# Optimization experiments

Hardware: AMD Instinct MI355X
Metric: run time of the kernel (lower is better)

## Reference

```python
import jax, jax.numpy as jnp
import numpy as np


def setup_inputs() -> dict:
    key = jax.random.key(0)
    k1, k2 = jax.random.split(key)
    B, Q, C, H, W = 2, 100, 151, 128, 128
    pred_logits = jax.random.normal(k1, (B, Q, C), dtype=jnp.float32)
    pred_masks = jax.random.normal(k2, (B, Q, H, W), dtype=jnp.float32)
    return {"pred_logits": pred_logits, "pred_masks": pred_masks, "out_size": 512}


def reference(pred_logits, pred_masks, out_size):
    B, Q, C = pred_logits.shape
    # class_scores[b,q,c] * mask_probs[b,q,h,w] summed over q == contraction bqc,bqhw->bchw
    class_scores = jax.nn.softmax(pred_logits, axis=-1)
    mask_probs = jax.nn.sigmoid(pred_masks)
    seg = jnp.einsum('bqc,bqhw->bchw', class_scores, mask_probs)
    seg = seg[:, 1:, :, :]  # drop background class 0
    # bilinear, half-pixel centers == torch align_corners=False
    seg = jax.image.resize(seg, (B, C - 1, out_size, out_size), method='bilinear')
    return seg
```

## Files before the change

kernel.cpp:

```cpp
#include <hip/hip_runtime.h>
#include <hip/hip_bf16.h>
#include <math.h>

#define NCLS 151
#define NQ   100
#define NB   2
#define HW   16384
#define NCO  150
#define OUTW 512
#define KPAD 128
#define CPAD 160
#define CBLK 32
#define AROW 136
#define BROW 72
#define SROW 130

using short8  = __attribute__((ext_vector_type(8))) short;
using short4v = __attribute__((ext_vector_type(4))) short;
using f32x4   = __attribute__((ext_vector_type(4))) float;

static __device__ __forceinline__ ushort f2bf(float x) {
    union { float f; unsigned u; } v; v.f = x;
    unsigned r = v.u + 0x7fff + ((v.u >> 16) & 1);
    return (ushort)(r >> 16);
}

__global__ __launch_bounds__(64) void softmax_k(const float* __restrict__ logits,
                                                ushort* __restrict__ scoresT) {
    int q = blockIdx.x & 127;
    int b = blockIdx.x >> 7;
    int lane = threadIdx.x;
    ushort* A = scoresT + (size_t)b * CPAD * KPAD;

    if (q >= NQ) {
        A[lane * KPAD + q] = 0;
        A[(lane + 64) * KPAD + q] = 0;
        if (lane < 32) A[(lane + 128) * KPAD + q] = 0;
        return;
    }

    const float* in = logits + (size_t)(b * NQ + q) * NCLS;
    float v0 = in[lane];
    float v1 = in[lane + 64];
    float v2 = (lane < NCLS - 128) ? in[lane + 128] : -1e30f;

    float m = fmaxf(fmaxf(v0, v1), v2);
    #pragma unroll
    for (int o = 32; o; o >>= 1) m = fmaxf(m, __shfl_xor(m, o));

    float e0 = __expf(v0 - m);
    float e1 = __expf(v1 - m);
    float e2 = (lane < NCLS - 128) ? __expf(v2 - m) : 0.f;

    float s = e0 + e1 + e2;
    #pragma unroll
    for (int o = 32; o; o >>= 1) s += __shfl_xor(s, o);

    float inv = 1.f / s;
    if (lane >= 1) A[(lane - 1) * KPAD + q] = f2bf(e0 * inv);
    A[(lane + 63) * KPAD + q] = f2bf(e1 * inv);
    if (lane < 23)       A[(lane + 127) * KPAD + q] = f2bf(e2 * inv);
    else if (lane < 33)  A[(lane + 127) * KPAD + q] = 0;
}

__global__ __launch_bounds__(512, 4) void fused_k(const float* __restrict__ masks,
                                                  const ushort* __restrict__ scoresT,
                                                  float* __restrict__ out) {
    __shared__ __align__(16) ushort s_a[CBLK][AROW];
    __shared__ __align__(16) char uni[256 * BROW * 2];
    ushort (*s_bt)[BROW] = (ushort(*)[BROW])uni;
    float* s_seg = (float*)uni;

    int r   = blockIdx.x;
    int b   = blockIdx.y / 5;
    int cs  = blockIdx.y % 5;
    int tid = threadIdx.x;
    int r1  = min(r + 1, 127);
    int wid = tid >> 6, lane = tid & 63;
    int pr = lane & 15, kg = lane >> 4;

    {
        const float4* asrc = (const float4*)(scoresT + (size_t)(b * CPAD + cs * CBLK) * KPAD);
        float4 av = asrc[tid];
        int c = tid >> 4, kc = tid & 15;
        *(float4*)&s_a[c][kc * 8] = av;
    }

    f32x4 acc[2][2];
    #pragma unroll
    for (int ct = 0; ct < 2; ++ct)
        #pragma unroll
        for (int nt = 0; nt < 2; ++nt) acc[ct][nt] = (f32x4){0.f, 0.f, 0.f, 0.f};

    const float* mb = masks + (size_t)b * NQ * HW;

    #pragma unroll
    for (int kc2 = 0; kc2 < 2; ++kc2) {
        #pragma unroll
        for (int i0 = 0; i0 < 4096; i0 += 512) {
            int i = i0 + tid;
            int p = i & 255, kk4 = i >> 8;
            int gpix = ((p < 128) ? r : r1) * 128 + (p & 127);
            short4v sv;
            #pragma unroll
            for (int e = 0; e < 4; ++e) {
                int gk = kc2 * 64 + kk4 * 4 + e;
                float s = 0.f;
                if (gk < NQ) {
                    float x = mb[(size_t)gk * HW + gpix];
                    s = 1.f / (1.f + __expf(-x));
                }
                sv[e] = (short)f2bf(s);
            }
            *(short4v*)&s_bt[p][kk4 * 4] = sv;
        }
        __syncthreads();

        #pragma unroll
        for (int ks = 0; ks < 2; ++ks) {
            short8 b0 = *(const short8*)&s_bt[wid * 32 + pr][ks * 32 + kg * 8];
            short8 b1 = *(const short8*)&s_bt[wid * 32 + 16 + pr][ks * 32 + kg * 8];
            #pragma unroll
            for (int ct = 0; ct < 2; ++ct) {
                short8 af = *(const short8*)&s_a[ct * 16 + pr][kc2 * 64 + ks * 32 + kg * 8];
                acc[ct][0] = __builtin_amdgcn_mfma_f32_16x16x32_bf16(af, b0, acc[ct][0], 0, 0, 0);
                acc[ct][1] = __builtin_amdgcn_mfma_f32_16x16x32_bf16(af, b1, acc[ct][1], 0, 0, 0);
            }
        }
        __syncthreads();
    }

    #pragma unroll
    for (int ct = 0; ct < 2; ++ct)
        #pragma unroll
        for (int nt = 0; nt < 2; ++nt) {
            int p = wid * 32 + nt * 16 + pr;
            int rs = p >> 7, px = p & 127;
            #pragma unroll
            for (int j = 0; j < 4; ++j) {
                int c = ct * 16 + kg * 4 + j;
                s_seg[(rs * CBLK + c) * SROW + px] = acc[ct][nt][j];
            }
        }
    __syncthreads();

    int cbase = cs * CBLK;
    for (int it = tid; it < CBLK * 128; it += 512) {
        int k = it & 127;
        int c = it >> 7;
        int cg = cbase + c;
        if (cg >= NCO) break;
        int km = max(k - 1, 0), kp = min(k + 1, 127);
        const float* s0 = &s_seg[c * SROW];
        const float* s1 = &s_seg[(CBLK + c) * SROW];
        float a0 = s0[km], a1 = s0[k], a2 = s0[kp];
        float b0 = s1[km], b1 = s1[k], b2 = s1[kp];

        float t0 = a0 + 0.625f * (a1 - a0);
        float t1 = a0 + 0.875f * (a1 - a0);
        float t2 = a1 + 0.125f * (a2 - a1);
        float t3 = a1 + 0.375f * (a2 - a1);
        float u0 = b0 + 0.625f * (b1 - b0);
        float u1 = b0 + 0.875f * (b1 - b0);
        float u2 = b1 + 0.125f * (b2 - b1);
        float u3 = b1 + 0.375f * (b2 - b1);

        float* op = out + (size_t)(b * NCO + cg) * (OUTW * OUTW) + 4 * k;

        if (r == 0) {
            f32x4 o = {t0, t1, t2, t3};
            __builtin_nontemporal_store(o, (f32x4*)(op));
            __builtin_nontemporal_store(o, (f32x4*)(op + OUTW));
        }
        int nr = (r == 127) ? 2 : 4;
        #pragma unroll
        for (int ri = 0; ri < 4; ++ri) {
            if (ri >= nr) break;
            float fh = 0.125f + 0.25f * (float)ri;
            int h = 4 * r + 2 + ri;
            f32x4 o;
            o.x = t0 + fh * (u0 - t0);
            o.y = t1 + fh * (u1 - t1);
            o.z = t2 + fh * (u2 - t2);
            o.w = t3 + fh * (u3 - t3);
            __builtin_nontemporal_store(o, (f32x4*)(op + (size_t)h * OUTW));
        }
    }
}

extern "C" void kernel_launch(void* const* d_in, const int* in_sizes, int n_in,
                              void* d_out, int out_size, void* d_ws, size_t ws_size,
                              hipStream_t stream) {
    const float* logits = (const float*)d_in[0];
    const float* masks  = (const float*)d_in[1];
    float* out = (float*)d_out;

    ushort* scoresT = (ushort*)d_ws;

    softmax_k<<<dim3(NB * 128), dim3(64), 0, stream>>>(logits, scoresT);
    fused_k<<<dim3(128, NB * 5), dim3(512), 0, stream>>>(masks, scoresT, out);
}
```

Measured before the change: 72.29 us.

## Compute sigmoid mask tile once per block and loop over all class chunks

Each block now loads and sigmoids the two mask rows for all 128 queries once, keeps them in LDS, and loops over the five class chunks internally, where previously five separate blocks each redid that load and sigmoid. This removes the 5x redundant global mask reads and transcendental work. In exchange the grid shrinks from 1280 to 256 blocks, LDS use per block grows (occupancy hint lowered to 2), and the output write phase is serialized within each block, which may reduce parallelism for the store-bound resize.

```diff
diff --git a/kernel.cpp b/kernel.cpp
--- a/kernel.cpp
+++ b/kernel.cpp
@@ -12,7 +12,7 @@
 #define CPAD 160
 #define CBLK 32
 #define AROW 136
-#define BROW 72
+#define BROW 136
 #define SROW 130
 
 using short8  = __attribute__((ext_vector_type(8))) short;
@@ -63,48 +63,42 @@
     else if (lane < 33)  A[(lane + 127) * KPAD + q] = 0;
 }
 
-__global__ __launch_bounds__(512, 4) void fused_k(const float* __restrict__ masks,
+__global__ __launch_bounds__(512, 2) void fused_k(const float* __restrict__ masks,
                                                   const ushort* __restrict__ scoresT,
                                                   float* __restrict__ out) {
-    __shared__ __align__(16) ushort s_a[CBLK][AROW];
-    __shared__ __align__(16) char uni[256 * BROW * 2];
-    ushort (*s_bt)[BROW] = (ushort(*)[BROW])uni;
-    float* s_seg = (float*)uni;
+    __shared__ __align__(16) ushort s_a[CPAD][AROW];
+    __shared__ __align__(16) ushort s_bt[256][BROW];
+    __shared__ float s_seg[2][CBLK][SROW];
 
     int r   = blockIdx.x;
-    int b   = blockIdx.y / 5;
-    int cs  = blockIdx.y % 5;
+    int b   = blockIdx.y;
     int tid = threadIdx.x;
     int r1  = min(r + 1, 127);
     int wid = tid >> 6, lane = tid & 63;
     int pr = lane & 15, kg = lane >> 4;
 
     {
-        const float4* asrc = (const float4*)(scoresT + (size_t)(b * CPAD + cs * CBLK) * KPAD);
-        float4 av = asrc[tid];
-        int c = tid >> 4, kc = tid & 15;
-        *(float4*)&s_a[c][kc * 8] = av;
-    }
-
-    f32x4 acc[2][2];
-    #pragma unroll
-    for (int ct = 0; ct < 2; ++ct)
-        #pragma unroll
-        for (int nt = 0; nt < 2; ++nt) acc[ct][nt] = (f32x4){0.f, 0.f, 0.f, 0.f};
-
-    const float* mb = masks + (size_t)b * NQ * HW;
-
-    #pragma unroll
-    for (int kc2 = 0; kc2 < 2; ++kc2) {
-        #pragma unroll
-        for (int i0 = 0; i0 < 4096; i0 += 512) {
+        const float4* asrc = (const float4*)(scoresT + (size_t)b * CPAD * KPAD);
+        #pragma unroll
+        for (int j = 0; j < 5; ++j) {
+            int i = tid + j * 512;
+            float4 v = asrc[i];
+            int c = i >> 4, kc = i & 15;
+            *(float4*)&s_a[c][kc * 8] = v;
+        }
+    }
+
+    {
+        const float* mb = masks + (size_t)b * NQ * HW;
+        #pragma unroll
+        for (int i0 = 0; i0 < 8192; i0 += 512) {
             int i = i0 + tid;
             int p = i & 255, kk4 = i >> 8;
             int gpix = ((p < 128) ? r : r1) * 128 + (p & 127);
             short4v sv;
             #pragma unroll
             for (int e = 0; e < 4; ++e) {
-                int gk = kc2 * 64 + kk4 * 4 + e;
+                int gk = kk4 * 4 + e;
                 float s = 0.f;
                 if (gk < NQ) {
                     float x = mb[(size_t)gk * HW + gpix];
@@ -114,76 +108,85 @@
             }
             *(short4v*)&s_bt[p][kk4 * 4] = sv;
         }
-        __syncthreads();
-
-        #pragma unroll
-        for (int ks = 0; ks < 2; ++ks) {
+    }
+    __syncthreads();
+
+    for (int cs = 0; cs < 5; ++cs) {
+        f32x4 acc[2][2];
+        #pragma unroll
+        for (int ct = 0; ct < 2; ++ct)
+            #pragma unroll
+            for (int nt = 0; nt < 2; ++nt) acc[ct][nt] = (f32x4){0.f, 0.f, 0.f, 0.f};
+
+        #pragma unroll
+        for (int ks = 0; ks < 4; ++ks) {
             short8 b0 = *(const short8*)&s_bt[wid * 32 + pr][ks * 32 + kg * 8];
             short8 b1 = *(const short8*)&s_bt[wid * 32 + 16 + pr][ks * 32 + kg * 8];
             #pragma unroll
             for (int ct = 0; ct < 2; ++ct) {
-                short8 af = *(const short8*)&s_a[ct * 16 + pr][kc2 * 64 + ks * 32 + kg * 8];
+                short8 af = *(const short8*)&s_a[cs * CBLK + ct * 16 + pr][ks * 32 + kg * 8];
                 acc[ct][0] = __builtin_amdgcn_mfma_f32_16x16x32_bf16(af, b0, acc[ct][0], 0, 0, 0);
                 acc[ct][1] = __builtin_amdgcn_mfma_f32_16x16x32_bf16(af, b1, acc[ct][1], 0, 0, 0);
             }
         }
+
         __syncthreads();
-    }
-
-    #pragma unroll
-    for (int ct = 0; ct < 2; ++ct)
-        #pragma unroll
-        for (int nt = 0; nt < 2; ++nt) {
-            int p = wid * 32 + nt * 16 + pr;
-            int rs = p >> 7, px = p & 127;
-            #pragma unroll
-            for (int j = 0; j < 4; ++j) {
-                int c = ct * 16 + kg * 4 + j;
-                s_seg[(rs * CBLK + c) * SROW + px] = acc[ct][nt][j];
-            }
-        }
-    __syncthreads();
-
-    int cbase = cs * CBLK;
-    for (int it = tid; it < CBLK * 128; it += 512) {
-        int k = it & 127;
-        int c = it >> 7;
-        int cg = cbase + c;
-        if (cg >= NCO) break;
-        int km = max(k - 1, 0), kp = min(k + 1, 127);
-        const float* s0 = &s_seg[c * SROW];
-        const float* s1 = &s_seg[(CBLK + c) * SROW];
-        float a0 = s0[km], a1 = s0[k], a2 = s0[kp];
-        float b0 = s1[km], b1 = s1[k], b2 = s1[kp];
-
-        float t0 = a0 + 0.625f * (a1 - a0);
-        float t1 = a0 + 0.875f * (a1 - a0);
-        float t2 = a1 + 0.125f * (a2 - a1);
-        float t3 = a1 + 0.375f * (a2 - a1);
-        float u0 = b0 + 0.625f * (b1 - b0);
-        float u1 = b0 + 0.875f * (b1 - b0);
-        float u2 = b1 + 0.125f * (b2 - b1);
-        float u3 = b1 + 0.375f * (b2 - b1);
-
-        float* op = out + (size_t)(b * NCO + cg) * (OUTW * OUTW) + 4 * k;
-
-        if (r == 0) {
-            f32x4 o = {t0, t1, t2, t3};
-            __builtin_nontemporal_store(o, (f32x4*)(op));
-            __builtin_nontemporal_store(o, (f32x4*)(op + OUTW));
-        }
-        int nr = (r == 127) ? 2 : 4;
-        #pragma unroll
-        for (int ri = 0; ri < 4; ++ri) {
-            if (ri >= nr) break;
-            float fh = 0.125f + 0.25f * (float)ri;
-            int h = 4 * r + 2 + ri;
-            f32x4 o;
-            o.x = t0 + fh * (u0 - t0);
-            o.y = t1 + fh * (u1 - t1);
-            o.z = t2 + fh * (u2 - t2);
-            o.w = t3 + fh * (u3 - t3);
-            __builtin_nontemporal_store(o, (f32x4*)(op + (size_t)h * OUTW));
+
+        #pragma unroll
+        for (int ct = 0; ct < 2; ++ct)
+            #pragma unroll
+            for (int nt = 0; nt < 2; ++nt) {
+                int p = wid * 32 + nt * 16 + pr;
+                int rs = p >> 7, px = p & 127;
+                #pragma unroll
+                for (int j = 0; j < 4; ++j) {
+                    int c = ct * 16 + kg * 4 + j;
+                    s_seg[rs][c][px] = acc[ct][nt][j];
+                }
+            }
+        __syncthreads();
+
+        int cbase = cs * CBLK;
+        for (int it = tid; it < CBLK * 128; it += 512) {
+            int k = it & 127;
+            int c = it >> 7;
+            int cg = cbase + c;
+            if (cg >= NCO) break;
+            int km = max(k - 1, 0), kp = min(k + 1, 127);
+            const float* s0 = s_seg[0][c];
+            const float* s1 = s_seg[1][c];
+            float a0 = s0[km], a1 = s0[k], a2 = s0[kp];
+            float b0 = s1[km], b1 = s1[k], b2 = s1[kp];
+
+            float t0 = a0 + 0.625f * (a1 - a0);
+            float t1 = a0 + 0.875f * (a1 - a0);
+            float t2 = a1 + 0.125f * (a2 - a1);
+            float t3 = a1 + 0.375f * (a2 - a1);
+            float u0 = b0 + 0.625f * (b1 - b0);
+            float u1 = b0 + 0.875f * (b1 - b0);
+            float u2 = b1 + 0.125f * (b2 - b1);
+            float u3 = b1 + 0.375f * (b2 - b1);
+
+            float* op = out + (size_t)(b * NCO + cg) * (OUTW * OUTW) + 4 * k;
+
+            if (r == 0) {
+                f32x4 o = {t0, t1, t2, t3};
+                __builtin_nontemporal_store(o, (f32x4*)(op));
+                __builtin_nontemporal_store(o, (f32x4*)(op + OUTW));
+            }
+            int nr = (r == 127) ? 2 : 4;
+            #pragma unroll
+            for (int ri = 0; ri < 4; ++ri) {
+                if (ri >= nr) break;
+                float fh = 0.125f + 0.25f * (float)ri;
+                int h = 4 * r + 2 + ri;
+                f32x4 o;
+                o.x = t0 + fh * (u0 - t0);
+                o.y = t1 + fh * (u1 - t1);
+                o.z = t2 + fh * (u2 - t2);
+                o.w = t3 + fh * (u3 - t3);
+                __builtin_nontemporal_store(o, (f32x4*)(op + (size_t)h * OUTW));
+            }
         }
     }
 }
@@ -198,5 +201,5 @@
     ushort* scoresT = (ushort*)d_ws;
 
     softmax_k<<<dim3(NB * 128), dim3(64), 0, stream>>>(logits, scoresT);
-    fused_k<<<dim3(128, NB * 5), dim3(512), 0, stream>>>(masks, scoresT, out);
-}
+    fused_k<<<dim3(128, NB), dim3(512), 0, stream>>>(masks, scoresT, out);
+}
```

Result: no change. 72.09 us (-0.3%).
